# Kernel tuning notes

Measured on AMD Instinct MI355X. Metric: run time of the kernel, lower is better.

## Reference

```python
import jax, jax.numpy as jnp
import numpy as np

B, IN_DIM, HID, N_WIRES = 8192, 2048, 2048, 8


def setup_inputs() -> dict:
    key = jax.random.key(0)
    ks = jax.random.split(key, 12)
    fan_in = IN_DIM + HID
    w_scale = 1.0 / np.sqrt(fan_in)  # ~ nn.Linear default init scale
    mk_w = lambda k: jax.random.normal(k, (N_WIRES, fan_in), jnp.float32) * w_scale
    mk_b = lambda k: jax.random.normal(k, (N_WIRES,), jnp.float32) * w_scale
    return {
        "x": jax.random.normal(ks[0], (B, IN_DIM), jnp.float32),
        "hx": jax.random.normal(ks[1], (B, HID), jnp.float32),
        "cx": jax.random.normal(ks[2], (B, HID), jnp.float32),
        "Wf": mk_w(ks[3]), "bf": mk_b(ks[4]),
        "Wi": mk_w(ks[5]), "bi": mk_b(ks[6]),
        "Wg": mk_w(ks[7]), "bg": mk_b(ks[8]),
        "Wo": mk_w(ks[9]), "bo": mk_b(ks[10]),
    }


def reference(x, hx, cx, Wf, bf, Wi, bi, Wg, bg, Wo, bo):
    combined = jnp.concatenate([x, hx], axis=1)  # [B, IN+HID]
    # Exact expectation of the RX-only circuit: E[#zeros - #ones] = sum_i cos(angle_i)
    q_exp = lambda W, b: jnp.sum(jnp.cos(combined @ W.T + b))
    f = jax.nn.sigmoid(q_exp(Wf, bf))
    i = jax.nn.sigmoid(q_exp(Wi, bi))
    g = jnp.tanh(q_exp(Wg, bg))
    o = jax.nn.sigmoid(q_exp(Wo, bo))
    cx_new = f * cx + i * g
    hx_new = o * jnp.tanh(cx_new)
    return hx_new, cx_new
```

## Files before the change

kernel.cpp:

```cpp
#include <hip/hip_runtime.h>
#include <hip/hip_bf16.h>
#include <cstdint>
#include <cstddef>

#define B_ROWS 8192
#define KDIM   4096
#define IN_DIM 2048
#define HIDDEN 2048
#define NJ     32
#define KC     4
#define CHUNK  (KDIM / KC)
#define BK     64
#define SUBT   (CHUNK / BK)
#define MROWS  16
#define TPB1   64
#define NBUF   4

typedef __bf16 bf16x8 __attribute__((ext_vector_type(8)));
typedef __bf16 bf16x4 __attribute__((ext_vector_type(4)));
typedef float  f32x4  __attribute__((ext_vector_type(4)));

__device__ __forceinline__ bf16x8 cvt8(f32x4 a, f32x4 b) {
    bf16x8 r;
    r[0] = (__bf16)a.x; r[1] = (__bf16)a.y; r[2] = (__bf16)a.z; r[3] = (__bf16)a.w;
    r[4] = (__bf16)b.x; r[5] = (__bf16)b.y; r[6] = (__bf16)b.z; r[7] = (__bf16)b.w;
    return r;
}

__device__ __forceinline__ void gload_lds16(const void* g, void* lds) {
    __builtin_amdgcn_global_load_lds(
        (const __attribute__((address_space(1))) void*)g,
        (__attribute__((address_space(3))) void*)lds, 16, 0, 0);
}

extern "C" __global__ __launch_bounds__(256)
void w_pack(const float* __restrict__ Wf, const float* __restrict__ Wi,
            const float* __restrict__ Wg, const float* __restrict__ Wo,
            __bf16* __restrict__ Wb, float* __restrict__ q)
{
    if (blockIdx.x == 0 && threadIdx.x < 4) q[threadIdx.x] = 0.f;

    const int t    = blockIdx.x * 256 + threadIdx.x;
    const int idx4 = t << 2;
    const int j    = idx4 >> 12;
    const int k    = idx4 & (KDIM - 1);
    const float* W = (j < 8) ? Wf : (j < 16) ? Wi : (j < 24) ? Wg : Wo;
    f32x4 v = *reinterpret_cast<const f32x4*>(W + (size_t)(j & 7) * KDIM + k);
    bf16x4 b;
    b[0] = (__bf16)v.x; b[1] = (__bf16)v.y; b[2] = (__bf16)v.z; b[3] = (__bf16)v.w;
    *reinterpret_cast<bf16x4*>(Wb + idx4) = b;
}

extern "C" __global__ __launch_bounds__(TPB1)
void p1_mfma(const float* __restrict__ x, const float* __restrict__ hx,
             const __bf16* __restrict__ Wb, float* __restrict__ Spart)
{
    __shared__ float  Abuf[NBUF][MROWS * BK];
    __shared__ __bf16 Bbuf[NBUF][NJ * BK];

    const int bid  = blockIdx.x;
    const int kc   = bid & (KC - 1);
    const int mb   = bid >> 2;
    const int lane = threadIdx.x & 63;
    const int lrow = lane & 15;
    const int rowblk = mb * MROWS;
    const int k0   = kc * CHUNK;

    const float* Aglob = (kc < 2)
        ? (x  + (size_t)rowblk * IN_DIM + k0)
        : (hx + (size_t)rowblk * HIDDEN + (k0 - IN_DIM));
    const __bf16* Bglob = Wb + k0;

    int aOff[4];
#pragma unroll
    for (int p = 0; p < 4; ++p) {
        const int r  = p * 4 + (lane >> 4);
        const int cs = (lane & 15) ^ (r & 7);
        aOff[p] = r * 2048 + cs * 4;
    }
    int bOff[4];
#pragma unroll
    for (int i = 0; i < 4; ++i) {
        const int j = i * 8 + (lane >> 3);
        bOff[i] = j * KDIM + (((lane & 7) ^ (j & 7)) * 8);
    }

    int offA0[2], offA1[2], offB0[2], offB1[2];
#pragma unroll
    for (int st = 0; st < 2; ++st) {
        const int cu = st * 8 + (lane >> 4) * 2;
        offA0[st] = lrow * 256 + (((cu + 0) ^ (lane & 7)) * 16);
        offA1[st] = lrow * 256 + (((cu + 1) ^ (lane & 7)) * 16);
        const int cb = st * 4 + (lane >> 4);
        offB0[st] = lrow * 128        + ((cb ^ (lrow & 7)) * 16);
        offB1[st] = (lrow + 16) * 128 + ((cb ^ (lrow & 7)) * 16);
    }

    f32x4 acc0 = {0.f, 0.f, 0.f, 0.f};
    f32x4 acc1 = {0.f, 0.f, 0.f, 0.f};

    auto issue = [&](int s) {
        const int b = s & (NBUF - 1);
#pragma unroll
        for (int p = 0; p < 4; ++p)
            gload_lds16(Aglob + aOff[p] + s * BK, &Abuf[b][p * 256]);
#pragma unroll
        for (int i = 0; i < 4; ++i)
            gload_lds16(Bglob + bOff[i] + s * BK, &Bbuf[b][i * 512]);
    };
    auto compute = [&](int s) {
        const int b = s & (NBUF - 1);
        const char* Ab = (const char*)&Abuf[b][0];
        const char* Bb = (const char*)&Bbuf[b][0];
#pragma unroll
        for (int st = 0; st < 2; ++st) {
            f32x4 a0 = *reinterpret_cast<const f32x4*>(Ab + offA0[st]);
            f32x4 a1 = *reinterpret_cast<const f32x4*>(Ab + offA1[st]);
            bf16x8 af = cvt8(a0, a1);
            bf16x8 b0 = *reinterpret_cast<const bf16x8*>(Bb + offB0[st]);
            bf16x8 b1 = *reinterpret_cast<const bf16x8*>(Bb + offB1[st]);
            acc0 = __builtin_amdgcn_mfma_f32_16x16x32_bf16(af, b0, acc0, 0, 0, 0);
            acc1 = __builtin_amdgcn_mfma_f32_16x16x32_bf16(af, b1, acc1, 0, 0, 0);
        }
    };

    issue(0);
    issue(1);
    issue(2);
#pragma unroll
    for (int s = 0; s < SUBT; ++s) {
        if (s + 3 < SUBT) issue(s + 3);
        if (s < SUBT - 3)
            asm volatile("s_waitcnt vmcnt(24)" ::: "memory");
        else if (s == SUBT - 3)
            asm volatile("s_waitcnt vmcnt(16)" ::: "memory");
        else if (s == SUBT - 2)
            asm volatile("s_waitcnt vmcnt(8)" ::: "memory");
        else
            asm volatile("s_waitcnt vmcnt(0)" ::: "memory");
        __builtin_amdgcn_sched_barrier(0);
        compute(s);
    }

    float* sp = Spart + ((size_t)kc * B_ROWS + rowblk) * NJ;
    const int m0 = (lane >> 4) * 4;
#pragma unroll
    for (int r = 0; r < 4; ++r) {
        sp[(size_t)(m0 + r) * NJ + lrow]      = acc0[r];
        sp[(size_t)(m0 + r) * NJ + 16 + lrow] = acc1[r];
    }
}

extern "C" __global__ __launch_bounds__(256)
void p2_cos_reduce(const float* __restrict__ Spart,
                   const float* __restrict__ bf, const float* __restrict__ bi,
                   const float* __restrict__ bg, const float* __restrict__ bo,
                   float* __restrict__ q)
{
    __shared__ float ql[4];
    if (threadIdx.x < 4) ql[threadIdx.x] = 0.f;
    __syncthreads();

    const int t    = blockIdx.x * 256 + threadIdx.x;
    const int j    = t & 31;
    const int gate = j >> 3;
    const float* Bp = (gate == 0) ? bf : (gate == 1) ? bi : (gate == 2) ? bg : bo;
    const float bj = Bp[j & 7];

    float accg = 0.f;
#pragma unroll
    for (int i = 0; i < 4; ++i) {
        const int row = (t >> 5) + i * 2048;
        float s = 0.f;
#pragma unroll
        for (int kc = 0; kc < KC; ++kc)
            s += Spart[((size_t)kc * B_ROWS + row) * NJ + j];
        accg += cosf(s + bj);
    }

    accg += __shfl_xor(accg, 1, 64);
    accg += __shfl_xor(accg, 2, 64);
    accg += __shfl_xor(accg, 4, 64);
    if ((threadIdx.x & 7) == 0) atomicAdd(&ql[gate], accg);
    __syncthreads();
    if (threadIdx.x < 4) atomicAdd(&q[threadIdx.x], ql[threadIdx.x]);
}

extern "C" __global__ __launch_bounds__(256)
void p3_elementwise(const float* __restrict__ cx, const float* __restrict__ q,
                    float* __restrict__ out)
{
    const float qf = q[0], qi = q[1], qg = q[2], qo = q[3];
    const float f  = 1.f / (1.f + expf(-qf));
    const float ii = 1.f / (1.f + expf(-qi));
    const float g  = tanhf(qg);
    const float o  = 1.f / (1.f + expf(-qo));
    const float ig = ii * g;

    const size_t N  = (size_t)B_ROWS * HIDDEN;
    const size_t N4 = N >> 2;
    const f32x4* cx4 = (const f32x4*)cx;
    f32x4* outh = (f32x4*)out;
    f32x4* outc = (f32x4*)(out + N);

    for (size_t idx = (size_t)blockIdx.x * blockDim.x + threadIdx.x; idx < N4;
         idx += (size_t)gridDim.x * blockDim.x) {
        f32x4 c = cx4[idx];
        f32x4 cn, hn;
        cn.x = fmaf(f, c.x, ig);
        cn.y = fmaf(f, c.y, ig);
        cn.z = fmaf(f, c.z, ig);
        cn.w = fmaf(f, c.w, ig);
        hn.x = o * tanhf(cn.x);
        hn.y = o * tanhf(cn.y);
        hn.z = o * tanhf(cn.z);
        hn.w = o * tanhf(cn.w);
        __builtin_nontemporal_store(cn, outc + idx);
        __builtin_nontemporal_store(hn, outh + idx);
    }
}

extern "C" void kernel_launch(void* const* d_in, const int* in_sizes, int n_in,
                              void* d_out, int out_size, void* d_ws, size_t ws_size,
                              hipStream_t stream)
{
    const float* x  = (const float*)d_in[0];
    const float* hx = (const float*)d_in[1];
    const float* cx = (const float*)d_in[2];
    const float* Wf = (const float*)d_in[3];
    const float* bf = (const float*)d_in[4];
    const float* Wi = (const float*)d_in[5];
    const float* bi = (const float*)d_in[6];
    const float* Wg = (const float*)d_in[7];
    const float* bg = (const float*)d_in[8];
    const float* Wo = (const float*)d_in[9];
    const float* bo = (const float*)d_in[10];
    float* out = (float*)d_out;

    float*   Spart = (float*)d_ws;
    __bf16*  Wb    = (__bf16*)(Spart + (size_t)KC * B_ROWS * NJ);
    float*   q     = (float*)(Wb + (size_t)NJ * KDIM);

    w_pack<<<dim3(128), dim3(256), 0, stream>>>(Wf, Wi, Wg, Wo, Wb, q);
    p1_mfma<<<dim3(512 * KC), dim3(TPB1), 0, stream>>>(x, hx, Wb, Spart);
    p2_cos_reduce<<<dim3(256), dim3(256), 0, stream>>>(Spart, bf, bi, bg, bo, q);
    p3_elementwise<<<dim3(2048), dim3(256), 0, stream>>>(cx, q, out);
}
```

Baseline: 69.82 us.

## Fuse weight bf16 conversion into GEMM and replace atomics with per-block partials

Removes the separate w_pack kernel. The GEMM now streams fp32 weights straight from the four gate matrices into LDS and converts them to bf16 in registers. To fit the larger fp32 B tiles in LDS, the pipeline depth drops from 4 to 3 buffers, and the vmcnt waits are adjusted to match. The global atomic accumulation of q is replaced with per-block partial sums that p3 reduces at startup, which also removes the need for a zeroing pass. The trade-offs are that weight bytes read per GEMM block double, each block does more conversion work, and the shallower prefetch hides less latency.

```diff
diff --git a/kernel.cpp b/kernel.cpp
--- a/kernel.cpp
+++ b/kernel.cpp
@@ -14,10 +14,9 @@
 #define SUBT   (CHUNK / BK)
 #define MROWS  16
 #define TPB1   64
-#define NBUF   4
+#define NBUF   3
 
 typedef __bf16 bf16x8 __attribute__((ext_vector_type(8)));
-typedef __bf16 bf16x4 __attribute__((ext_vector_type(4)));
 typedef float  f32x4  __attribute__((ext_vector_type(4)));
 
 __device__ __forceinline__ bf16x8 cvt8(f32x4 a, f32x4 b) {
@@ -33,30 +32,14 @@
         (__attribute__((address_space(3))) void*)lds, 16, 0, 0);
 }
 
-extern "C" __global__ __launch_bounds__(256)
-void w_pack(const float* __restrict__ Wf, const float* __restrict__ Wi,
-            const float* __restrict__ Wg, const float* __restrict__ Wo,
-            __bf16* __restrict__ Wb, float* __restrict__ q)
-{
-    if (blockIdx.x == 0 && threadIdx.x < 4) q[threadIdx.x] = 0.f;
-
-    const int t    = blockIdx.x * 256 + threadIdx.x;
-    const int idx4 = t << 2;
-    const int j    = idx4 >> 12;
-    const int k    = idx4 & (KDIM - 1);
-    const float* W = (j < 8) ? Wf : (j < 16) ? Wi : (j < 24) ? Wg : Wo;
-    f32x4 v = *reinterpret_cast<const f32x4*>(W + (size_t)(j & 7) * KDIM + k);
-    bf16x4 b;
-    b[0] = (__bf16)v.x; b[1] = (__bf16)v.y; b[2] = (__bf16)v.z; b[3] = (__bf16)v.w;
-    *reinterpret_cast<bf16x4*>(Wb + idx4) = b;
-}
-
 extern "C" __global__ __launch_bounds__(TPB1)
 void p1_mfma(const float* __restrict__ x, const float* __restrict__ hx,
-             const __bf16* __restrict__ Wb, float* __restrict__ Spart)
-{
-    __shared__ float  Abuf[NBUF][MROWS * BK];
-    __shared__ __bf16 Bbuf[NBUF][NJ * BK];
+             const float* __restrict__ Wf, const float* __restrict__ Wi,
+             const float* __restrict__ Wg, const float* __restrict__ Wo,
+             float* __restrict__ Spart)
+{
+    __shared__ float Abuf[NBUF][MROWS * BK];
+    __shared__ float Bbuf[NBUF][NJ * BK];
 
     const int bid  = blockIdx.x;
     const int kc   = bid & (KC - 1);
@@ -69,7 +52,6 @@
     const float* Aglob = (kc < 2)
         ? (x  + (size_t)rowblk * IN_DIM + k0)
         : (hx + (size_t)rowblk * HIDDEN + (k0 - IN_DIM));
-    const __bf16* Bglob = Wb + k0;
 
     int aOff[4];
 #pragma unroll
@@ -78,64 +60,69 @@
         const int cs = (lane & 15) ^ (r & 7);
         aOff[p] = r * 2048 + cs * 4;
     }
-    int bOff[4];
-#pragma unroll
-    for (int i = 0; i < 4; ++i) {
-        const int j = i * 8 + (lane >> 3);
-        bOff[i] = j * KDIM + (((lane & 7) ^ (j & 7)) * 8);
-    }
-
-    int offA0[2], offA1[2], offB0[2], offB1[2];
+    const float* Wsrc[8] = {Wf, Wf, Wi, Wi, Wg, Wg, Wo, Wo};
+    int bOffp[8];
+#pragma unroll
+    for (int sl = 0; sl < 8; ++sl) {
+        const int j  = sl * 4 + (lane >> 4);
+        const int j7 = j & 7;
+        bOffp[sl] = j7 * KDIM + (((lane & 15) ^ j7) * 4);
+    }
+
+    int offA0[2], offA1[2], offB00[2], offB01[2], offB10[2], offB11[2];
 #pragma unroll
     for (int st = 0; st < 2; ++st) {
         const int cu = st * 8 + (lane >> 4) * 2;
-        offA0[st] = lrow * 256 + (((cu + 0) ^ (lane & 7)) * 16);
-        offA1[st] = lrow * 256 + (((cu + 1) ^ (lane & 7)) * 16);
-        const int cb = st * 4 + (lane >> 4);
-        offB0[st] = lrow * 128        + ((cb ^ (lrow & 7)) * 16);
-        offB1[st] = (lrow + 16) * 128 + ((cb ^ (lrow & 7)) * 16);
+        offA0[st]  = lrow * 256 + (((cu + 0) ^ (lane & 7)) * 16);
+        offA1[st]  = lrow * 256 + (((cu + 1) ^ (lane & 7)) * 16);
+        offB00[st] = lrow * 256        + (((cu + 0) ^ (lane & 7)) * 16);
+        offB01[st] = lrow * 256        + (((cu + 1) ^ (lane & 7)) * 16);
+        offB10[st] = (lrow + 16) * 256 + (((cu + 0) ^ (lane & 7)) * 16);
+        offB11[st] = (lrow + 16) * 256 + (((cu + 1) ^ (lane & 7)) * 16);
     }
 
     f32x4 acc0 = {0.f, 0.f, 0.f, 0.f};
     f32x4 acc1 = {0.f, 0.f, 0.f, 0.f};
 
     auto issue = [&](int s) {
-        const int b = s & (NBUF - 1);
+        const int b = s % NBUF;
 #pragma unroll
         for (int p = 0; p < 4; ++p)
-            gload_lds16(Aglob + aOff[p] + s * BK, &Abuf[b][p * 256]);
-#pragma unroll
-        for (int i = 0; i < 4; ++i)
-            gload_lds16(Bglob + bOff[i] + s * BK, &Bbuf[b][i * 512]);
+            gload_lds16(Aglob + aOff[p] + s * BK, (char*)&Abuf[b][0] + p * 1024);
+#pragma unroll
+        for (int sl = 0; sl < 8; ++sl)
+            gload_lds16(Wsrc[sl] + bOffp[sl] + k0 + s * BK,
+                        (char*)&Bbuf[b][0] + sl * 1024);
     };
     auto compute = [&](int s) {
-        const int b = s & (NBUF - 1);
+        const int b = s % NBUF;
         const char* Ab = (const char*)&Abuf[b][0];
         const char* Bb = (const char*)&Bbuf[b][0];
 #pragma unroll
         for (int st = 0; st < 2; ++st) {
-            f32x4 a0 = *reinterpret_cast<const f32x4*>(Ab + offA0[st]);
-            f32x4 a1 = *reinterpret_cast<const f32x4*>(Ab + offA1[st]);
-            bf16x8 af = cvt8(a0, a1);
-            bf16x8 b0 = *reinterpret_cast<const bf16x8*>(Bb + offB0[st]);
-            bf16x8 b1 = *reinterpret_cast<const bf16x8*>(Bb + offB1[st]);
-            acc0 = __builtin_amdgcn_mfma_f32_16x16x32_bf16(af, b0, acc0, 0, 0, 0);
-            acc1 = __builtin_amdgcn_mfma_f32_16x16x32_bf16(af, b1, acc1, 0, 0, 0);
+            f32x4 a0  = *reinterpret_cast<const f32x4*>(Ab + offA0[st]);
+            f32x4 a1  = *reinterpret_cast<const f32x4*>(Ab + offA1[st]);
+            f32x4 w00 = *reinterpret_cast<const f32x4*>(Bb + offB00[st]);
+            f32x4 w01 = *reinterpret_cast<const f32x4*>(Bb + offB01[st]);
+            f32x4 w10 = *reinterpret_cast<const f32x4*>(Bb + offB10[st]);
+            f32x4 w11 = *reinterpret_cast<const f32x4*>(Bb + offB11[st]);
+            bf16x8 af  = cvt8(a0, a1);
+            bf16x8 bf0 = cvt8(w00, w01);
+            bf16x8 bf1 = cvt8(w10, w11);
+            acc0 = __builtin_amdgcn_mfma_f32_16x16x32_bf16(af, bf0, acc0, 0, 0, 0);
+            acc1 = __builtin_amdgcn_mfma_f32_16x16x32_bf16(af, bf1, acc1, 0, 0, 0);
         }
     };
 
     issue(0);
     issue(1);
-    issue(2);
 #pragma unroll
     for (int s = 0; s < SUBT; ++s) {
-        if (s + 3 < SUBT) issue(s + 3);
-        if (s < SUBT - 3)
+        if (s + 2 < SUBT) issue(s + 2);
+        if (s < SUBT - 2)
             asm volatile("s_waitcnt vmcnt(24)" ::: "memory");
-        else if (s == SUBT - 3)
-            asm volatile("s_waitcnt vmcnt(16)" ::: "memory");
         else if (s == SUBT - 2)
-            asm volatile("s_waitcnt vmcnt(8)" ::: "memory");
+            asm volatile("s_waitcnt vmcnt(12)" ::: "memory");
         else
             asm volatile("s_waitcnt vmcnt(0)" ::: "memory");
         __builtin_amdgcn_sched_barrier(0);
@@ -155,7 +142,7 @@
 void p2_cos_reduce(const float* __restrict__ Spart,
                    const float* __restrict__ bf, const float* __restrict__ bi,
                    const float* __restrict__ bg, const float* __restrict__ bo,
-                   float* __restrict__ q)
+                   float* __restrict__ qpart)
 {
     __shared__ float ql[4];
     if (threadIdx.x < 4) ql[threadIdx.x] = 0.f;
@@ -183,14 +170,36 @@
     accg += __shfl_xor(accg, 4, 64);
     if ((threadIdx.x & 7) == 0) atomicAdd(&ql[gate], accg);
     __syncthreads();
-    if (threadIdx.x < 4) atomicAdd(&q[threadIdx.x], ql[threadIdx.x]);
+    if (threadIdx.x < 4) qpart[blockIdx.x * 4 + threadIdx.x] = ql[threadIdx.x];
 }
 
 extern "C" __global__ __launch_bounds__(256)
-void p3_elementwise(const float* __restrict__ cx, const float* __restrict__ q,
+void p3_elementwise(const float* __restrict__ cx, const float* __restrict__ qpart,
                     float* __restrict__ out)
 {
-    const float qf = q[0], qi = q[1], qg = q[2], qo = q[3];
+    __shared__ float qs[4][4];
+    const int tid  = threadIdx.x;
+    const int wave = tid >> 6;
+    const int lane = tid & 63;
+
+    f32x4 qp = *reinterpret_cast<const f32x4*>(qpart + tid * 4);
+#pragma unroll
+    for (int m = 1; m <= 32; m <<= 1) {
+        qp.x += __shfl_xor(qp.x, m, 64);
+        qp.y += __shfl_xor(qp.y, m, 64);
+        qp.z += __shfl_xor(qp.z, m, 64);
+        qp.w += __shfl_xor(qp.w, m, 64);
+    }
+    if (lane == 0) {
+        qs[wave][0] = qp.x; qs[wave][1] = qp.y;
+        qs[wave][2] = qp.z; qs[wave][3] = qp.w;
+    }
+    __syncthreads();
+    const float qf = qs[0][0] + qs[1][0] + qs[2][0] + qs[3][0];
+    const float qi = qs[0][1] + qs[1][1] + qs[2][1] + qs[3][1];
+    const float qg = qs[0][2] + qs[1][2] + qs[2][2] + qs[3][2];
+    const float qo = qs[0][3] + qs[1][3] + qs[2][3] + qs[3][3];
+
     const float f  = 1.f / (1.f + expf(-qf));
     const float ii = 1.f / (1.f + expf(-qi));
     const float g  = tanhf(qg);
@@ -203,7 +212,7 @@
     f32x4* outh = (f32x4*)out;
     f32x4* outc = (f32x4*)(out + N);
 
-    for (size_t idx = (size_t)blockIdx.x * blockDim.x + threadIdx.x; idx < N4;
+    for (size_t idx = (size_t)blockIdx.x * blockDim.x + tid; idx < N4;
          idx += (size_t)gridDim.x * blockDim.x) {
         f32x4 c = cx4[idx];
         f32x4 cn, hn;
@@ -237,12 +246,12 @@
     const float* bo = (const float*)d_in[10];
     float* out = (float*)d_out;
 
-    float*   Spart = (float*)d_ws;
-    __bf16*  Wb    = (__bf16*)(Spart + (size_t)KC * B_ROWS * NJ);
-    float*   q     = (float*)(Wb + (size_t)NJ * KDIM);
-
-    w_pack<<<dim3(128), dim3(256), 0, stream>>>(Wf, Wi, Wg, Wo, Wb, q);
-    p1_mfma<<<dim3(512 * KC), dim3(TPB1), 0, stream>>>(x, hx, Wb, Spart);
-    p2_cos_reduce<<<dim3(256), dim3(256), 0, stream>>>(Spart, bf, bi, bg, bo, q);
-    p3_elementwise<<<dim3(2048), dim3(256), 0, stream>>>(cx, q, out);
-}
+    float* Spart = (float*)d_ws;
+    float* qpart = Spart + (size_t)KC * B_ROWS * NJ;
+
+    p1_mfma<<<dim3(512 * KC), dim3(TPB1), 0, stream>>>(
+        x, hx, Wf, Wi, Wg, Wo, Spart);
+    p2_cos_reduce<<<dim3(256), dim3(256), 0, stream>>>(
+        Spart, bf, bi, bg, bo, qpart);
+    p3_elementwise<<<dim3(2048), dim3(256), 0, stream>>>(cx, qpart, out);
+}
```

Result: faster. 63.29 us (-9.3%).
